# Optimization experiments

Measured on AMD Instinct MI355X. Metric: run time of the kernel, lower is better.

The kernel has to match this reference:

```python
import jax, jax.numpy as jnp
import numpy as np

DN = ('NCHW', 'HWIO', 'NCHW')  # NCHW data, HWIO kernels


def conv3x3(x, k, b=None):
    # 'same'-padded 3x3 conv, stride 1, NCHW layout
    y = jax.lax.conv_general_dilated(x, k, (1, 1), 'SAME', dimension_numbers=DN)
    if b is not None:
        y = y + b[None, :, None, None]
    return y


def setup_inputs() -> dict:
    B, T, C, H, W = 4, 4, 256, 30, 40
    CA = 256  # nb_filters_att (== nb_filters_out == nb_filters_in per SAM)
    key = jax.random.key(0)
    ks = jax.random.split(key, 10)
    s = 0.05  # small init scale so gates don't saturate
    x = jax.random.normal(ks[0], (B, T, C, H, W), dtype=jnp.float32)
    # attention convs
    Wa = jax.random.normal(ks[1], (3, 3, C, CA), dtype=jnp.float32) * s
    ba = jnp.zeros((CA,), dtype=jnp.float32)
    Ua = jax.random.normal(ks[2], (3, 3, C, CA), dtype=jnp.float32) * s
    bua = jnp.zeros((CA,), dtype=jnp.float32)
    # V_a has attentive_init='zero' in the original; random here for a nontrivial baseline
    Va = jax.random.normal(ks[3], (3, 3, CA, 1), dtype=jnp.float32) * s
    # gate convs: stack i,f,c,o along output channels (same math as 4 separate 3x3 convs)
    Wx = jax.random.normal(ks[4], (3, 3, C, 4 * C), dtype=jnp.float32) * s
    bx = jnp.zeros((4 * C,), dtype=jnp.float32)
    Uh = jax.random.normal(ks[5], (3, 3, C, 4 * C), dtype=jnp.float32) * s
    bh = jnp.zeros((4 * C,), dtype=jnp.float32)
    return {"x": x, "Wa": Wa, "ba": ba, "Ua": Ua, "bua": bua, "Va": Va,
            "Wx": Wx, "bx": bx, "Uh": Uh, "bh": bh}


def reference(x, Wa, ba, Ua, bua, Va, Wx, bx, Uh, bh):
    B, T, C, H, W = x.shape
    # initial h and c: sum over the time axis (K.sum(x, axis=1))
    h0 = jnp.sum(x, axis=1)
    c0 = h0

    def step(carry, xt):
        h, c = carry
        # conv-based spatial attention
        e = conv3x3(jnp.tanh(conv3x3(h, Wa, ba) + conv3x3(xt, Ua, bua)), Va)  # [B,1,H,W]
        a = jax.nn.softmax(e.reshape(B, -1), axis=-1).reshape(B, 1, H, W)
        x_tilde = xt * a  # broadcast over channels
        # fused gate convs: i | f | c | o along channel axis
        g = conv3x3(x_tilde, Wx, bx) + conv3x3(h, Uh, bh)  # [B,4C,H,W]
        gi, gf, gc, go = jnp.split(g, 4, axis=1)
        i = jax.nn.sigmoid(gi)
        f = jax.nn.sigmoid(gf)
        o = jax.nn.sigmoid(go)
        c_new = f * c + i * jnp.tanh(gc)
        h_new = o * jnp.tanh(c_new)
        return (h_new, c_new), None

    (h_last, _), _ = jax.lax.scan(step, (h0, c0), jnp.swapaxes(x, 0, 1))
    return h_last  # [B, C_out, H, W], the last RNN output
```

## Files before the change

### kernel.cpp

```cpp
#include <hip/hip_runtime.h>
#include <math.h>

#define BB 4
#define TT 4
#define CC 256
#define HH 30
#define WW 40
#define HWS (HH*WW)
#define CHW (CC*HWS)
#define CHW4 (CHW/4)
#define PL 170

typedef __attribute__((ext_vector_type(8))) _Float16 half8;
typedef __attribute__((ext_vector_type(4))) float f32x4;

__global__ void init_hc(const float* __restrict__ x,
                        float* __restrict__ h, float* __restrict__ c) {
    int id = blockIdx.x * 256 + threadIdx.x;
    if (id >= BB * CHW4) return;
    int b = id / CHW4;
    int rem = id - b * CHW4;
    const f32x4* xv = (const f32x4*)x;
    f32x4 s = {0.f, 0.f, 0.f, 0.f};
#pragma unroll
    for (int t = 0; t < TT; ++t)
        s += xv[((size_t)b * TT + t) * CHW4 + rem];
    ((f32x4*)h)[id] = s;
    ((f32x4*)c)[id] = s;
}

__global__ void pack_weights(const float* __restrict__ W1,
                             const float* __restrict__ W2,
                             _Float16* __restrict__ wt, int Cout) {
    int idx = blockIdx.x * 256 + threadIdx.x;
    if (idx >= 4608 * Cout) return;
    int k = idx / Cout;
    int n = idx - k * Cout;
    float v = (k < 2304) ? W1[(size_t)k * Cout + n]
                         : W2[(size_t)(k - 2304) * Cout + n];
    wt[((size_t)(k >> 3) * Cout + n) * 8 + (k & 7)] = (_Float16)v;
}

template<int NW, int NZ, int NY, int ZT>
__global__ __launch_bounds__(256, 3) void conv_mfma(
    const float* __restrict__ in0, long bs0, const float* __restrict__ scale,
    const float* __restrict__ in1, long bs1,
    const _Float16* __restrict__ wt,
    const float* __restrict__ b1, const float* __restrict__ b2,
    float* __restrict__ out, int Cout)
{
    constexpr int NK = 8 / NZ;
    __shared__ alignas(16) _Float16 s_a[2][4 * PL * 8];

    const int tid = threadIdx.x;
    const int l = tid & 63, wv = tid >> 6;
    const int q = l >> 4, r = l & 15;

    const int lin = blockIdx.x;
    const int xcd = lin & 7;
    const int idx = lin >> 3;
    const int second = (idx >= 60) ? 1 : 0;
    const int sl = xcd * 2 + second;
    const int mb = idx - second * 60;
    const int zz = sl / NY;
    const int yy = sl - zz * NY;

    const int b = mb / 15;
    const int pix0 = (mb % 15) * 80;
    const int y0 = (mb % 15) * 2;
    const int n0 = yy * (4 * NW * 16) + wv * (NW * 16);
    const int src = zz / NZ;
    const int ci_start = (zz % NZ) * (CC / NZ);
    const int kgb0 = src * 288 + (ci_start >> 3);

    const float* inp = (src ? in1 + (size_t)b * bs1 : in0 + (size_t)b * bs0)
                       + (size_t)ci_start * HWS;
    const float* scl = (src == 0) ? scale : nullptr;

    bool iv[3], pv[3];
    const float* pj[3];
    float sc[3];
    int ldsoff[3];
#pragma unroll
    for (int j = 0; j < 3; ++j) {
        int item = tid + j * 256;
        iv[j] = item < 672;
        int it = iv[j] ? item : 0;
        int cig = it / 168;
        int pix = it - cig * 168;
        int row = pix / 42;
        int px = pix - row * 42;
        int xx = px - 1, yy2 = y0 + row - 1;
        pv[j] = iv[j] && xx >= 0 && xx < WW && yy2 >= 0 && yy2 < HH;
        pj[j] = inp + (size_t)(cig * 8) * HWS + yy2 * WW + xx;
        sc[j] = 1.f;
        if (scl && pv[j]) sc[j] = scl[(size_t)b * HWS + yy2 * WW + xx];
        ldsoff[j] = (cig * PL + pix) * 8;
    }

    f32x4 acc[5][NW];
#pragma unroll
    for (int nt = 0; nt < NW; ++nt) {
        int co = n0 + nt * 16 + r;
        float bias = (zz == 0) ? (b1[co] + b2[co]) : 0.f;
        f32x4 bv = {bias, bias, bias, bias};
#pragma unroll
        for (int mt = 0; mt < 5; ++mt) acc[mt][nt] = bv;
    }

    int hbase[5];
#pragma unroll
    for (int mt = 0; mt < 5; ++mt) {
        int p = mt * 16 + r;
        int ry = p / 40;
        int rx = p - ry * 40;
        hbase[mt] = ry * 42 + rx;
    }

    float sr[3][8];
    auto stage_issue = [&](int kk) {
#pragma unroll
        for (int j = 0; j < 3; ++j) if (pv[j]) {
            const float* p0 = pj[j] + (size_t)kk * 32 * HWS;
#pragma unroll
            for (int t = 0; t < 8; ++t) sr[j][t] = p0[(size_t)t * HWS];
        }
    };
    auto stage_write = [&](int kk) {
#pragma unroll
        for (int j = 0; j < 3; ++j) if (iv[j]) {
            half8 hv = {0, 0, 0, 0, 0, 0, 0, 0};
            if (pv[j]) {
#pragma unroll
                for (int t = 0; t < 8; ++t)
                    hv[t] = (_Float16)(sr[j][t] * sc[j]);
            }
            *(half8*)&s_a[kk & 1][ldsoff[j]] = hv;
        }
    };

    const half8* wp = (const half8*)wt;
    half8 w0[NW], w1[NW], w2[NW], w3[NW];

#define WLOAD(SLOT, TAP) do {                                              \
    const int kg_ = kgb0 + k * 4 + (TAP) * 32 + q;                         \
    _Pragma("unroll")                                                      \
    for (int nt = 0; nt < NW; ++nt)                                        \
        SLOT[nt] = wp[(size_t)kg_ * Cout + n0 + nt * 16 + r];              \
} while (0)

#define CTAP(SLOT, TAP) do {                                               \
    constexpr int dy_ = (TAP) / 3, dx_ = (TAP) % 3;                        \
    _Pragma("unroll")                                                      \
    for (int mt = 0; mt < 5; ++mt) {                                       \
        half8 af = *(const half8*)&s_a[k & 1]                              \
            [(q * PL + hbase[mt] + dy_ * 42 + dx_) * 8];                   \
        _Pragma("unroll")                                                  \
        for (int nt = 0; nt < NW; ++nt)                                    \
            acc[mt][nt] = __builtin_amdgcn_mfma_f32_16x16x32_f16(          \
                af, SLOT[nt], acc[mt][nt], 0, 0, 0);                       \
    }                                                                      \
} while (0)

    stage_issue(0);
    stage_write(0);

#pragma unroll
    for (int k = 0; k < NK; ++k) {
        WLOAD(w0, 0); WLOAD(w1, 1); WLOAD(w2, 2);
        if (k + 1 < NK) stage_issue(k + 1);
        __syncthreads();
        __builtin_amdgcn_s_setprio(1);
        WLOAD(w3, 3); CTAP(w0, 0);
        WLOAD(w0, 4); CTAP(w1, 1);
        WLOAD(w1, 5); CTAP(w2, 2);
        WLOAD(w2, 6); CTAP(w3, 3);
        WLOAD(w3, 7); CTAP(w0, 4);
        WLOAD(w0, 8); CTAP(w1, 5);
        __builtin_amdgcn_s_setprio(0);
        if (k + 1 < NK) stage_write(k + 1);
        __builtin_amdgcn_s_setprio(1);
        CTAP(w2, 6);
        CTAP(w3, 7);
        CTAP(w0, 8);
        __builtin_amdgcn_s_setprio(0);
    }
#undef WLOAD
#undef CTAP

    out += (size_t)zz * BB * Cout * HWS;
#pragma unroll
    for (int mt = 0; mt < 5; ++mt) {
#pragma unroll
        for (int nt = 0; nt < NW; ++nt) {
            int co = n0 + nt * 16 + r;
            int p = pix0 + mt * 16 + q * 4;
            *(f32x4*)&out[((size_t)b * Cout + co) * HWS + p] = acc[mt][nt];
        }
    }
}

__global__ void add_tanh4(const float* __restrict__ a0,
                          float* __restrict__ o, int n4) {
    int id = blockIdx.x * 256 + threadIdx.x;
    if (id >= n4) return;
    const f32x4* av = (const f32x4*)a0;
    f32x4 s = av[id] + av[id + (size_t)n4] + av[id + 2 * (size_t)n4]
            + av[id + 3 * (size_t)n4];
    f32x4 rr;
#pragma unroll
    for (int j = 0; j < 4; ++j) rr[j] = tanhf(s[j]);
    ((f32x4*)o)[id] = rr;
}

__global__ __launch_bounds__(256) void att_e_part(
    const float* __restrict__ att, const float* __restrict__ Va,
    float* __restrict__ part)
{
    __shared__ float red[4][64];
    const int lane = threadIdx.x & 63, wv = threadIdx.x >> 6;
    const int p = blockIdx.x * 64 + lane;
    const int b = blockIdx.y, ch = blockIdx.z;
    const bool valid = (p < HWS);
    const int pc = valid ? p : 0;
    const int y = pc / WW, x = pc - (pc / WW) * WW;

    float acc = 0.f;
    if (valid) {
        const int ca0 = ch * 32 + wv * 8;
#pragma unroll
        for (int j = 0; j < 8; ++j) {
            const int ca = ca0 + j;
            const float* base = att + ((size_t)b * CC + ca) * HWS;
            const float* va = Va + ca;
#pragma unroll
            for (int dy = 0; dy < 3; ++dy) {
                int yy = y + dy - 1;
                if (yy < 0 || yy >= HH) continue;
#pragma unroll
                for (int dx = 0; dx < 3; ++dx) {
                    int xx = x + dx - 1;
                    if (xx < 0 || xx >= WW) continue;
                    acc = fmaf(base[yy * WW + xx], va[(dy * 3 + dx) * CC], acc);
                }
            }
        }
    }
    red[wv][lane] = acc;
    __syncthreads();
    if (wv == 0 && valid)
        part[((size_t)b * 8 + ch) * HWS + p] =
            red[0][lane] + red[1][lane] + red[2][lane] + red[3][lane];
}

__global__ __launch_bounds__(256) void softmax_kernel(
    const float* __restrict__ part, float* __restrict__ a)
{
    __shared__ float se[HWS];
    __shared__ float red[256];
    int b = blockIdx.x;
    int tid = threadIdx.x;

    for (int i = tid; i < HWS; i += 256) {
        float s = 0.f;
#pragma unroll
        for (int ch = 0; ch < 8; ++ch)
            s += part[((size_t)b * 8 + ch) * HWS + i];
        se[i] = s;
    }
    __syncthreads();

    float m = -1e30f;
    for (int i = tid; i < HWS; i += 256) m = fmaxf(m, se[i]);
    red[tid] = m;
    __syncthreads();
    for (int s = 128; s > 0; s >>= 1) {
        if (tid < s) red[tid] = fmaxf(red[tid], red[tid + s]);
        __syncthreads();
    }
    m = red[0];
    __syncthreads();

    float sum = 0.f;
    for (int i = tid; i < HWS; i += 256) {
        float v = expf(se[i] - m);
        se[i] = v;
        sum += v;
    }
    red[tid] = sum;
    __syncthreads();
    for (int s = 128; s > 0; s >>= 1) {
        if (tid < s) red[tid] += red[tid + s];
        __syncthreads();
    }
    float inv = 1.f / red[0];
    for (int i = tid; i < HWS; i += 256)
        a[(size_t)b * HWS + i] = se[i] * inv;
}

__global__ void gate_update(const float* __restrict__ g0, const float* __restrict__ g1,
                            float* __restrict__ c, float* __restrict__ h_out) {
    int id = blockIdx.x * 256 + threadIdx.x;
    if (id >= BB * CHW4) return;
    int b = id / CHW4;
    int rem = id - b * CHW4;
    const f32x4* g0v = (const f32x4*)g0;
    const f32x4* g1v = (const f32x4*)g1;
    size_t gb = (size_t)b * 4 * CHW4 + rem;
    f32x4 gi = g0v[gb] + g1v[gb];
    f32x4 gf = g0v[gb + CHW4] + g1v[gb + CHW4];
    f32x4 gc = g0v[gb + 2 * (size_t)CHW4] + g1v[gb + 2 * (size_t)CHW4];
    f32x4 go = g0v[gb + 3 * (size_t)CHW4] + g1v[gb + 3 * (size_t)CHW4];
    f32x4 cv = ((const f32x4*)c)[id];
    f32x4 cn, hn;
#pragma unroll
    for (int j = 0; j < 4; ++j) {
        float i_ = 1.f / (1.f + expf(-gi[j]));
        float f_ = 1.f / (1.f + expf(-gf[j]));
        float o_ = 1.f / (1.f + expf(-go[j]));
        float cc = f_ * cv[j] + i_ * tanhf(gc[j]);
        cn[j] = cc;
        hn[j] = o_ * tanhf(cc);
    }
    ((f32x4*)c)[id] = cn;
    ((f32x4*)h_out)[id] = hn;
}

extern "C" void kernel_launch(void* const* d_in, const int* in_sizes, int n_in,
                              void* d_out, int out_size, void* d_ws, size_t ws_size,
                              hipStream_t stream) {
    const float* x   = (const float*)d_in[0];
    const float* Wa  = (const float*)d_in[1];
    const float* ba  = (const float*)d_in[2];
    const float* Ua  = (const float*)d_in[3];
    const float* bua = (const float*)d_in[4];
    const float* Va  = (const float*)d_in[5];
    const float* Wx  = (const float*)d_in[6];
    const float* bx  = (const float*)d_in[7];
    const float* Uh  = (const float*)d_in[8];
    const float* bh  = (const float*)d_in[9];
    float* out = (float*)d_out;

    char* wsb = (char*)d_ws;
    const size_t NCHW = (size_t)BB * CHW;
    _Float16* wtg = (_Float16*)wsb;               wsb += (size_t)4608 * 1024 * 2;
    _Float16* wta = (_Float16*)wsb;               wsb += (size_t)4608 * 256 * 2;
    float* h0   = (float*)wsb;                    wsb += NCHW * 4;
    float* h1   = (float*)wsb;                    wsb += NCHW * 4;
    float* cb   = (float*)wsb;                    wsb += NCHW * 4;
    float* g01  = (float*)wsb;                    wsb += 8 * NCHW * 4;
    float* att  = (float*)wsb;                    wsb += NCHW * 4;
    float* part = (float*)wsb;                    wsb += (size_t)BB * 8 * HWS * 4;
    float* a    = (float*)wsb;
    float* att01 = g01;

    pack_weights<<<dim3((4608 * 1024 + 255) / 256), dim3(256), 0, stream>>>(
        Wx, Uh, wtg, 1024);
    pack_weights<<<dim3((4608 * 256 + 255) / 256), dim3(256), 0, stream>>>(
        Wa, Ua, wta, 256);

    const int n4 = BB * CHW4;
    init_hc<<<dim3((n4 + 255) / 256), dim3(256), 0, stream>>>(x, h0, cb);

    float* hbuf[2] = {h0, h1};
    const long XT_BS = (long)TT * CHW;
    const long H_BS  = (long)CHW;

    for (int t = 0; t < TT; ++t) {
        const float* xt = x + (size_t)t * CHW;
        float* hcur = hbuf[t & 1];
        float* hnext = (t == TT - 1) ? out : hbuf[(t + 1) & 1];

        conv_mfma<1, 2, 4, 4><<<dim3(960), dim3(256), 0, stream>>>(
            hcur, H_BS, nullptr, xt, XT_BS, wta, ba, bua, att01, 256);
        add_tanh4<<<dim3((n4 + 255) / 256), dim3(256), 0, stream>>>(
            att01, att, n4);

        att_e_part<<<dim3(19, BB, 8), dim3(256), 0, stream>>>(att, Va, part);
        softmax_kernel<<<dim3(BB), dim3(256), 0, stream>>>(part, a);

        conv_mfma<2, 1, 8, 2><<<dim3(960), dim3(256), 0, stream>>>(
            xt, XT_BS, a, hcur, H_BS, wtg, bx, bh, g01, 1024);

        gate_update<<<dim3((n4 + 255) / 256), dim3(256), 0, stream>>>(
            g01, g01 + 4 * NCHW, cb, hnext);
    }
}
```

Measured before the change: 616.3 us.

## Prepack activations to fp16 channel-grouped layout for conv staging

```diff
diff --git a/kernel.cpp b/kernel.cpp
--- a/kernel.cpp
+++ b/kernel.cpp
@@ -9,24 +9,62 @@
 #define HWS (HH*WW)
 #define CHW (CC*HWS)
 #define CHW4 (CHW/4)
-#define PL 170
+#define NCG 32
+#define PXS (NCG*HWS*8)
+#define PL 168
 
 typedef __attribute__((ext_vector_type(8))) _Float16 half8;
 typedef __attribute__((ext_vector_type(4))) float f32x4;
 
-__global__ void init_hc(const float* __restrict__ x,
-                        float* __restrict__ h, float* __restrict__ c) {
+__global__ void pack_x16(const float* __restrict__ x, _Float16* __restrict__ x16) {
     int id = blockIdx.x * 256 + threadIdx.x;
-    if (id >= BB * CHW4) return;
-    int b = id / CHW4;
-    int rem = id - b * CHW4;
-    const f32x4* xv = (const f32x4*)x;
-    f32x4 s = {0.f, 0.f, 0.f, 0.f};
-#pragma unroll
-    for (int t = 0; t < TT; ++t)
-        s += xv[((size_t)b * TT + t) * CHW4 + rem];
-    ((f32x4*)h)[id] = s;
-    ((f32x4*)c)[id] = s;
+    if (id >= BB * TT * NCG * HWS) return;
+    int p = id % HWS;
+    int cig = (id / HWS) % NCG;
+    int bt = id / (HWS * NCG);
+    const float* src = x + ((size_t)bt * CC + cig * 8) * HWS + p;
+    half8 hv;
+#pragma unroll
+    for (int j = 0; j < 8; ++j) hv[j] = (_Float16)src[(size_t)j * HWS];
+    *(half8*)&x16[(size_t)id * 8] = hv;
+}
+
+__global__ void init_hc(const float* __restrict__ x, _Float16* __restrict__ h16,
+                        float* __restrict__ c) {
+    int id = blockIdx.x * 256 + threadIdx.x;
+    if (id >= BB * NCG * HWS) return;
+    int p = id % HWS;
+    int cig = (id / HWS) % NCG;
+    int b = id / (HWS * NCG);
+    float s[8];
+#pragma unroll
+    for (int j = 0; j < 8; ++j) s[j] = 0.f;
+#pragma unroll
+    for (int t = 0; t < TT; ++t) {
+        const float* src = x + (((size_t)b * TT + t) * CC + cig * 8) * HWS + p;
+#pragma unroll
+        for (int j = 0; j < 8; ++j) s[j] += src[(size_t)j * HWS];
+    }
+    half8 hv;
+    float* cp = c + ((size_t)b * CC + cig * 8) * HWS + p;
+#pragma unroll
+    for (int j = 0; j < 8; ++j) { cp[(size_t)j * HWS] = s[j]; hv[j] = (_Float16)s[j]; }
+    *(half8*)&h16[(size_t)id * 8] = hv;
+}
+
+__global__ void xtilde_kernel(const float* __restrict__ xt, const float* __restrict__ a,
+                              _Float16* __restrict__ xt16) {
+    int id = blockIdx.x * 256 + threadIdx.x;
+    if (id >= BB * NCG * HWS) return;
+    int p = id % HWS;
+    int cig = (id / HWS) % NCG;
+    int b = id / (HWS * NCG);
+    float sc = a[(size_t)b * HWS + p];
+    const float* src = xt + ((size_t)b * TT * CC + cig * 8) * HWS + p;
+    half8 hv;
+#pragma unroll
+    for (int j = 0; j < 8; ++j) hv[j] = (_Float16)(src[(size_t)j * HWS] * sc);
+    *(half8*)&xt16[(size_t)id * 8] = hv;
 }
 
 __global__ void pack_weights(const float* __restrict__ W1,
@@ -42,9 +80,9 @@
 }
 
 template<int NW, int NZ, int NY, int ZT>
-__global__ __launch_bounds__(256, 3) void conv_mfma(
-    const float* __restrict__ in0, long bs0, const float* __restrict__ scale,
-    const float* __restrict__ in1, long bs1,
+__global__ __launch_bounds__(256, 4) void conv_mfma(
+    const _Float16* __restrict__ in0, long bs0,
+    const _Float16* __restrict__ in1, long bs1,
     const _Float16* __restrict__ wt,
     const float* __restrict__ b1, const float* __restrict__ b2,
     float* __restrict__ out, int Cout)
@@ -73,13 +111,10 @@
     const int ci_start = (zz % NZ) * (CC / NZ);
     const int kgb0 = src * 288 + (ci_start >> 3);
 
-    const float* inp = (src ? in1 + (size_t)b * bs1 : in0 + (size_t)b * bs0)
-                       + (size_t)ci_start * HWS;
-    const float* scl = (src == 0) ? scale : nullptr;
+    const _Float16* inp = src ? (in1 + (size_t)b * bs1) : (in0 + (size_t)b * bs0);
 
     bool iv[3], pv[3];
-    const float* pj[3];
-    float sc[3];
+    const _Float16* pj[3];
     int ldsoff[3];
 #pragma unroll
     for (int j = 0; j < 3; ++j) {
@@ -92,9 +127,7 @@
         int px = pix - row * 42;
         int xx = px - 1, yy2 = y0 + row - 1;
         pv[j] = iv[j] && xx >= 0 && xx < WW && yy2 >= 0 && yy2 < HH;
-        pj[j] = inp + (size_t)(cig * 8) * HWS + yy2 * WW + xx;
-        sc[j] = 1.f;
-        if (scl && pv[j]) sc[j] = scl[(size_t)b * HWS + yy2 * WW + xx];
+        pj[j] = inp + ((size_t)((ci_start >> 3) + cig) * HWS + yy2 * WW + xx) * 8;
         ldsoff[j] = (cig * PL + pix) * 8;
     }
 
@@ -117,24 +150,17 @@
         hbase[mt] = ry * 42 + rx;
     }
 
-    float sr[3][8];
+    half8 sr[3];
     auto stage_issue = [&](int kk) {
 #pragma unroll
-        for (int j = 0; j < 3; ++j) if (pv[j]) {
-            const float* p0 = pj[j] + (size_t)kk * 32 * HWS;
-#pragma unroll
-            for (int t = 0; t < 8; ++t) sr[j][t] = p0[(size_t)t * HWS];
-        }
+        for (int j = 0; j < 3; ++j) if (pv[j])
+            sr[j] = *(const half8*)(pj[j] + (size_t)kk * (4 * HWS * 8));
     };
     auto stage_write = [&](int kk) {
 #pragma unroll
         for (int j = 0; j < 3; ++j) if (iv[j]) {
             half8 hv = {0, 0, 0, 0, 0, 0, 0, 0};
-            if (pv[j]) {
-#pragma unroll
-                for (int t = 0; t < 8; ++t)
-                    hv[t] = (_Float16)(sr[j][t] * sc[j]);
-            }
+            if (pv[j]) hv = sr[j];
             *(half8*)&s_a[kk & 1][ldsoff[j]] = hv;
         }
     };
@@ -177,13 +203,11 @@
         WLOAD(w2, 6); CTAP(w3, 3);
         WLOAD(w3, 7); CTAP(w0, 4);
         WLOAD(w0, 8); CTAP(w1, 5);
-        __builtin_amdgcn_s_setprio(0);
-        if (k + 1 < NK) stage_write(k + 1);
-        __builtin_amdgcn_s_setprio(1);
         CTAP(w2, 6);
         CTAP(w3, 7);
         CTAP(w0, 8);
         __builtin_amdgcn_s_setprio(0);
+        if (k + 1 < NK) stage_write(k + 1);
     }
 #undef WLOAD
 #undef CTAP
@@ -299,31 +323,33 @@
 }
 
 __global__ void gate_update(const float* __restrict__ g0, const float* __restrict__ g1,
-                            float* __restrict__ c, float* __restrict__ h_out) {
+                            float* __restrict__ c, _Float16* __restrict__ h16,
+                            float* __restrict__ h32) {
     int id = blockIdx.x * 256 + threadIdx.x;
-    if (id >= BB * CHW4) return;
-    int b = id / CHW4;
-    int rem = id - b * CHW4;
-    const f32x4* g0v = (const f32x4*)g0;
-    const f32x4* g1v = (const f32x4*)g1;
-    size_t gb = (size_t)b * 4 * CHW4 + rem;
-    f32x4 gi = g0v[gb] + g1v[gb];
-    f32x4 gf = g0v[gb + CHW4] + g1v[gb + CHW4];
-    f32x4 gc = g0v[gb + 2 * (size_t)CHW4] + g1v[gb + 2 * (size_t)CHW4];
-    f32x4 go = g0v[gb + 3 * (size_t)CHW4] + g1v[gb + 3 * (size_t)CHW4];
-    f32x4 cv = ((const f32x4*)c)[id];
-    f32x4 cn, hn;
-#pragma unroll
-    for (int j = 0; j < 4; ++j) {
-        float i_ = 1.f / (1.f + expf(-gi[j]));
-        float f_ = 1.f / (1.f + expf(-gf[j]));
-        float o_ = 1.f / (1.f + expf(-go[j]));
-        float cc = f_ * cv[j] + i_ * tanhf(gc[j]);
-        cn[j] = cc;
-        hn[j] = o_ * tanhf(cc);
-    }
-    ((f32x4*)c)[id] = cn;
-    ((f32x4*)h_out)[id] = hn;
+    if (id >= BB * NCG * HWS) return;
+    int p = id % HWS;
+    int cig = (id / HWS) % NCG;
+    int b = id / (HWS * NCG);
+    const int ci0 = cig * 8;
+    half8 hv;
+#pragma unroll
+    for (int j = 0; j < 8; ++j) {
+        size_t base = ((size_t)b * 4 * CC + ci0 + j) * HWS + p;
+        float gi = g0[base] + g1[base];
+        float gf = g0[base + (size_t)CHW] + g1[base + (size_t)CHW];
+        float gc = g0[base + 2 * (size_t)CHW] + g1[base + 2 * (size_t)CHW];
+        float go = g0[base + 3 * (size_t)CHW] + g1[base + 3 * (size_t)CHW];
+        float i_ = 1.f / (1.f + expf(-gi));
+        float f_ = 1.f / (1.f + expf(-gf));
+        float o_ = 1.f / (1.f + expf(-go));
+        size_t cix = ((size_t)b * CC + ci0 + j) * HWS + p;
+        float cn = f_ * c[cix] + i_ * tanhf(gc);
+        c[cix] = cn;
+        float hn = o_ * tanhf(cn);
+        hv[j] = (_Float16)hn;
+        if (h32) h32[cix] = hn;
+    }
+    *(half8*)&h16[(size_t)id * 8] = hv;
 }
 
 extern "C" void kernel_launch(void* const* d_in, const int* in_sizes, int n_in,
@@ -343,10 +369,11 @@
 
     char* wsb = (char*)d_ws;
     const size_t NCHW = (size_t)BB * CHW;
-    _Float16* wtg = (_Float16*)wsb;               wsb += (size_t)4608 * 1024 * 2;
-    _Float16* wta = (_Float16*)wsb;               wsb += (size_t)4608 * 256 * 2;
-    float* h0   = (float*)wsb;                    wsb += NCHW * 4;
-    float* h1   = (float*)wsb;                    wsb += NCHW * 4;
+    _Float16* wtg  = (_Float16*)wsb;              wsb += (size_t)4608 * 1024 * 2;
+    _Float16* wta  = (_Float16*)wsb;              wsb += (size_t)4608 * 256 * 2;
+    _Float16* x16  = (_Float16*)wsb;              wsb += (size_t)BB * TT * PXS * 2;
+    _Float16* h16  = (_Float16*)wsb;              wsb += (size_t)BB * PXS * 2;
+    _Float16* xt16 = (_Float16*)wsb;              wsb += (size_t)BB * PXS * 2;
     float* cb   = (float*)wsb;                    wsb += NCHW * 4;
     float* g01  = (float*)wsb;                    wsb += 8 * NCHW * 4;
     float* att  = (float*)wsb;                    wsb += NCHW * 4;
@@ -358,31 +385,31 @@
         Wx, Uh, wtg, 1024);
     pack_weights<<<dim3((4608 * 256 + 255) / 256), dim3(256), 0, stream>>>(
         Wa, Ua, wta, 256);
-
-    const int n4 = BB * CHW4;
-    init_hc<<<dim3((n4 + 255) / 256), dim3(256), 0, stream>>>(x, h0, cb);
-
-    float* hbuf[2] = {h0, h1};
-    const long XT_BS = (long)TT * CHW;
-    const long H_BS  = (long)CHW;
+    pack_x16<<<dim3((BB * TT * NCG * HWS + 255) / 256), dim3(256), 0, stream>>>(
+        x, x16);
+
+    const int nblk = BB * NCG * HWS;
+    init_hc<<<dim3((nblk + 255) / 256), dim3(256), 0, stream>>>(x, h16, cb);
+
+    const int n4 = (int)(NCHW / 4);
 
     for (int t = 0; t < TT; ++t) {
-        const float* xt = x + (size_t)t * CHW;
-        float* hcur = hbuf[t & 1];
-        float* hnext = (t == TT - 1) ? out : hbuf[(t + 1) & 1];
-
         conv_mfma<1, 2, 4, 4><<<dim3(960), dim3(256), 0, stream>>>(
-            hcur, H_BS, nullptr, xt, XT_BS, wta, ba, bua, att01, 256);
+            h16, (long)PXS, x16 + (size_t)t * PXS, (long)TT * PXS,
+            wta, ba, bua, att01, 256);
         add_tanh4<<<dim3((n4 + 255) / 256), dim3(256), 0, stream>>>(
             att01, att, n4);
 
         att_e_part<<<dim3(19, BB, 8), dim3(256), 0, stream>>>(att, Va, part);
         softmax_kernel<<<dim3(BB), dim3(256), 0, stream>>>(part, a);
 
+        xtilde_kernel<<<dim3((nblk + 255) / 256), dim3(256), 0, stream>>>(
+            x + (size_t)t * CHW, a, xt16);
+
         conv_mfma<2, 1, 8, 2><<<dim3(960), dim3(256), 0, stream>>>(
-            xt, XT_BS, a, hcur, H_BS, wtg, bx, bh, g01, 1024);
-
-        gate_update<<<dim3((n4 + 255) / 256), dim3(256), 0, stream>>>(
-            g01, g01 + 4 * NCHW, cb, hnext);
-    }
-}
+            xt16, (long)PXS, h16, (long)PXS, wtg, bx, bh, g01, 1024);
+
+        gate_update<<<dim3((nblk + 255) / 256), dim3(256), 0, stream>>>(
+            g01, g01 + 4 * NCHW, cb, h16, (t == TT - 1) ? out : nullptr);
+    }
+}
```

Result: faster. 563.0 us (-8.6%).
